# Kernel tuning notes

Measured on AMD Instinct MI355X. Metric: run time of the kernel, lower is better.

## Reference

```python
import jax, jax.numpy as jnp
import numpy as np

ALPHA = 1.0
BETA = 1.0
N_TDA = 16      # n: points subsampled per diagram
Q = 2.0         # Wasserstein order
NN_SIZE = 5     # knn size (self + 4 neighbors)
RADIUS = 0.07
H = 0.03
EPS = 1e-12
B, N = 8, 4096


def _sqdist(a, b):
    # a: [..., M, 3], b: [..., K, 3] -> [..., M, K] squared Euclidean distances
    aa = jnp.sum(a * a, -1)[..., :, None]
    bb = jnp.sum(b * b, -1)[..., None, :]
    ab = jnp.einsum('...md,...kd->...mk', a, b)
    return aa + bb - 2.0 * ab


def _mst_deaths(pts):
    # H0 persistence of Vietoris-Rips complex: births all 0, finite deaths are
    # the edge weights of the MST of the complete graph (Prim's algorithm).
    n = pts.shape[0]
    d = jnp.sqrt(jnp.maximum(_sqdist(pts, pts), 0.0))  # [n, n]
    in_tree = jnp.zeros((n,), bool).at[0].set(True)
    mind = d[0]  # distance from each node to the current tree

    def step(carry, _):
        in_tree, mind = carry
        m = jnp.where(in_tree, jnp.inf, mind)
        j = jnp.argmin(m)
        w = m[j]
        in_tree = in_tree.at[j].set(True)
        mind = jnp.minimum(mind, d[j])
        return (in_tree, mind), w

    _, deaths = jax.lax.scan(step, (in_tree, mind), None, length=n - 1)
    return deaths  # [n-1]


def _forward(pred, gt, pcd_radius):
    b = pred.shape[0]
    # ---- EMD loss (nearest-neighbor surrogate of CUDA auction_match) ----
    cost = _sqdist(pred, gt)                              # [B, N, N]
    idx = jnp.argmin(cost, axis=-1)                       # [B, N]
    matched = jnp.take_along_axis(gt, idx[..., None], axis=1)
    d2 = jnp.mean(((pred - matched) ** 2).reshape(b, -1), axis=1, keepdims=True)
    emd = jnp.mean(d2 / pcd_radius)
    # ---- Repulsion loss ----
    dpp = _sqdist(pred, pred)                             # [B, N, N]
    _, knn = jax.lax.top_k(-dpp, NN_SIZE)                 # nearest incl. self
    knn = knn[:, :, 1:]                                   # drop self -> [B, N, 4]
    grouped = jax.vmap(lambda p, ix: p[ix])(pred, knn)    # [B, N, 4, 3]
    r2 = jnp.maximum(jnp.sum((grouped - pred[:, :, None, :]) ** 2, -1), EPS)
    dist = jnp.sqrt(r2)
    rep = jnp.mean((RADIUS - dist) * jnp.exp(-r2 / H ** 2))
    # ---- TDA loss (per-sample VR H0 diagram + q-Wasserstein) ----
    key = jax.random.key(42)
    kp, kg = jax.random.split(key)

    def sub(k, pts):
        ix = jax.random.permutation(k, pts.shape[0])[:N_TDA]
        return pts[ix]

    pred_s = jax.vmap(sub)(jax.random.split(kp, b), pred)  # [B, 16, 3]
    gt_s = jax.vmap(sub)(jax.random.split(kg, b), gt)
    dp = jnp.sort(jax.vmap(_mst_deaths)(pred_s), axis=-1)  # [B, 15]
    dg = jnp.sort(jax.vmap(_mst_deaths)(gt_s), axis=-1)
    wd = jnp.sum(jnp.abs(dp - dg) ** Q, axis=-1) ** (1.0 / Q)
    tda = jnp.mean(wd)
    return (emd * 100.0, rep * ALPHA, tda * BETA)


def setup_inputs() -> dict:
    key = jax.random.key(0)
    k1, k2, k3 = jax.random.split(key, 3)
    pred = jax.random.normal(k1, (B, N, 3), jnp.float32)
    gt = jax.random.normal(k2, (B, N, 3), jnp.float32)
    pcd_radius = jax.random.uniform(k3, (B, 1), jnp.float32) + 0.5
    return {"pred": pred, "gt": gt, "pcd_radius": pcd_radius}


def reference(pred, gt, pcd_radius):
    return _forward(pred, gt, pcd_radius)
```

## Files before the change

kernel.cpp:

```cpp
#include <hip/hip_runtime.h>
#include <cstdint>
#include <cmath>
#include <vector>
#include <algorithm>
#include <numeric>

#define B_SZ 8
#define N_PTS 4096
#define TBLK 256
#define NSPLIT 8
#define JTILE (N_PTS / NSPLIT)
#define ITILE 4
#define RCUT2 0.10f

struct TdaArgs { int idx[16][16]; };

#define WS_BT(p)   ((float*)(p))
#define WS_KNN(p)  ((unsigned short*)((char*)(p) + 0x100000))
#define WS_PART(p) ((double*)((char*)(p) + 0x380000))

__global__ __launch_bounds__(TBLK, 2)
void pair_kernel(const float* __restrict__ pred, const float* __restrict__ gt,
                 float* __restrict__ bt_out, unsigned short* __restrict__ knn_out) {
  __shared__ float4 sg[JTILE];

  const int tid  = threadIdx.x;
  const int xb   = blockIdx.x;
  const int b    = blockIdx.y;
  const int zz   = blockIdx.z;
  const int job  = zz >> 3;
  const int q    = zz & 7;
  const int jbase = q * JTILE;

  const float* src = (job == 0 ? gt : pred) + ((size_t)b * N_PTS + jbase) * 3;
  for (int j = tid; j < JTILE; j += TBLK) {
    float x = src[3 * j + 0];
    float y = src[3 * j + 1];
    float z = src[3 * j + 2];
    sg[j] = make_float4(x, y, z, -0.5f * fmaf(x, x, fmaf(y, y, z * z)));
  }

  const float* pb = pred + (size_t)b * N_PTS * 3;
  const int ibase = xb * (TBLK * ITILE) + tid;
  float px[ITILE], py[ITILE], pz[ITILE];
  #pragma unroll
  for (int ii = 0; ii < ITILE; ++ii) {
    int i = ibase + ii * TBLK;
    px[ii] = pb[3 * i + 0]; py[ii] = pb[3 * i + 1]; pz[ii] = pb[3 * i + 2];
  }
  __syncthreads();

  if (job == 0) {
    float bt[ITILE];
    #pragma unroll
    for (int ii = 0; ii < ITILE; ++ii) bt[ii] = -INFINITY;
    for (int j0 = 0; j0 < JTILE; j0 += 8) {
      float4 g[8];
      #pragma unroll
      for (int k = 0; k < 8; ++k) g[k] = sg[j0 + k];
      #pragma unroll
      for (int ii = 0; ii < ITILE; ++ii) {
        #pragma unroll
        for (int k = 0; k < 8; ++k) {
          float t = fmaf(px[ii], g[k].x, fmaf(py[ii], g[k].y, fmaf(pz[ii], g[k].z, g[k].w)));
          bt[ii] = fmaxf(bt[ii], t);
        }
      }
    }
    #pragma unroll
    for (int ii = 0; ii < ITILE; ++ii)
      bt_out[((size_t)q * B_SZ + b) * N_PTS + ibase + ii * TBLK] = bt[ii];
  } else {
    float t0[ITILE], t1[ITILE], t2[ITILE], t3[ITILE], t4[ITILE];
    int   i0v[ITILE], i1v[ITILE], i2v[ITILE], i3v[ITILE], i4v[ITILE];
    #pragma unroll
    for (int ii = 0; ii < ITILE; ++ii) {
      float pn = fmaf(px[ii], px[ii], fmaf(py[ii], py[ii], pz[ii] * pz[ii]));
      float tcut = 0.5f * (pn - RCUT2);
      t0[ii] = tcut; t1[ii] = tcut; t2[ii] = tcut; t3[ii] = tcut; t4[ii] = tcut;
      i0v[ii] = 0xFFFF; i1v[ii] = 0xFFFF; i2v[ii] = 0xFFFF; i3v[ii] = 0xFFFF; i4v[ii] = 0xFFFF;
    }
    #define INS(ii, tt, jj) { \
      t4[ii] = tt; i4v[ii] = jj; \
      if (t4[ii] > t3[ii]) { float f = t3[ii]; t3[ii] = t4[ii]; t4[ii] = f; int p_ = i3v[ii]; i3v[ii] = i4v[ii]; i4v[ii] = p_; } \
      if (t3[ii] > t2[ii]) { float f = t2[ii]; t2[ii] = t3[ii]; t3[ii] = f; int p_ = i2v[ii]; i2v[ii] = i3v[ii]; i3v[ii] = p_; } \
      if (t2[ii] > t1[ii]) { float f = t1[ii]; t1[ii] = t2[ii]; t2[ii] = f; int p_ = i1v[ii]; i1v[ii] = i2v[ii]; i2v[ii] = p_; } \
      if (t1[ii] > t0[ii]) { float f = t0[ii]; t0[ii] = t1[ii]; t1[ii] = f; int p_ = i0v[ii]; i0v[ii] = i1v[ii]; i1v[ii] = p_; } }
    for (int j0 = 0; j0 < JTILE; j0 += 4) {
      float4 g[4];
      #pragma unroll
      for (int k = 0; k < 4; ++k) g[k] = sg[j0 + k];
      #pragma unroll
      for (int ii = 0; ii < ITILE; ++ii) {
        #pragma unroll
        for (int k = 0; k < 4; ++k) {
          float t = fmaf(px[ii], g[k].x, fmaf(py[ii], g[k].y, fmaf(pz[ii], g[k].z, g[k].w)));
          if (t > t4[ii]) INS(ii, t, j0 + k);
        }
      }
    }
    #undef INS
    #pragma unroll
    for (int ii = 0; ii < ITILE; ++ii) {
      size_t base = (((size_t)q * B_SZ + b) * N_PTS + ibase + ii * TBLK) * 5;
      knn_out[base + 0] = (i0v[ii] == 0xFFFF) ? 0xFFFF : (unsigned short)(jbase + i0v[ii]);
      knn_out[base + 1] = (i1v[ii] == 0xFFFF) ? 0xFFFF : (unsigned short)(jbase + i1v[ii]);
      knn_out[base + 2] = (i2v[ii] == 0xFFFF) ? 0xFFFF : (unsigned short)(jbase + i2v[ii]);
      knn_out[base + 3] = (i3v[ii] == 0xFFFF) ? 0xFFFF : (unsigned short)(jbase + i3v[ii]);
      knn_out[base + 4] = (i4v[ii] == 0xFFFF) ? 0xFFFF : (unsigned short)(jbase + i4v[ii]);
    }
  }
}

__global__ __launch_bounds__(TBLK)
void merge_kernel(const float* __restrict__ pred,
                  const float* __restrict__ bt_in, const unsigned short* __restrict__ knn_in,
                  double* __restrict__ partials) {
  __shared__ double wred[2][TBLK / 64];
  const int tid = threadIdx.x;
  const int blk = blockIdx.x;
  const int b   = blk >> 4;
  const int i   = (blk & 15) * TBLK + tid;

  const float* pb = pred + (size_t)b * N_PTS * 3;
  const float px = pb[3 * i + 0], py = pb[3 * i + 1], pz = pb[3 * i + 2];
  const float pn = fmaf(px, px, fmaf(py, py, pz * pz));

  float bt = -INFINITY;
  #pragma unroll
  for (int q = 0; q < NSPLIT; ++q)
    bt = fmaxf(bt, bt_in[((size_t)q * B_SZ + b) * N_PTS + i]);
  double emd = (double)fmaf(-2.0f, bt, pn);

  float s0 = INFINITY, s1 = INFINITY, s2 = INFINITY, s3 = INFINITY;
  int   j0v = 0x7fffffff, j1v = 0x7fffffff, j2v = 0x7fffffff, j3v = 0x7fffffff;
  #pragma unroll
  for (int q = 0; q < NSPLIT; ++q) {
    const unsigned short* kn = knn_in + (((size_t)q * B_SZ + b) * N_PTS + i) * 5;
    #pragma unroll
    for (int c = 0; c < 5; ++c) {
      int v = kn[c];
      int idx = v & 0xFFF;
      float gx = pb[3 * idx + 0], gy = pb[3 * idx + 1], gz = pb[3 * idx + 2];
      float dx = px - gx, dy = py - gy, dz = pz - gz;
      float r2 = fmaf(dx, dx, fmaf(dy, dy, dz * dz));
      if (v >= 0xFFFF || idx == i) r2 = INFINITY;
      bool lt3 = (r2 < s3) || (r2 == s3 && idx < j3v);
      if (lt3) {
        s3 = r2; j3v = idx;
        if ((s3 < s2) || (s3 == s2 && j3v < j2v)) { float f = s2; s2 = s3; s3 = f; int p_ = j2v; j2v = j3v; j3v = p_; }
        if ((s2 < s1) || (s2 == s1 && j2v < j1v)) { float f = s1; s1 = s2; s2 = f; int p_ = j1v; j1v = j2v; j2v = p_; }
        if ((s1 < s0) || (s1 == s0 && j1v < j0v)) { float f = s0; s0 = s1; s1 = f; int p_ = j0v; j0v = j1v; j1v = p_; }
      }
    }
  }
  double rep = 0.0;
  {
    float rr[4] = { s0, s1, s2, s3 };
    #pragma unroll
    for (int k = 0; k < 4; ++k) {
      if (rr[k] < 1e30f) {
        float r2 = fmaxf(rr[k], 1e-12f);
        float dist = sqrtf(r2);
        rep += (double)((0.07f - dist) * expf(-r2 / 9.0e-4f));
      }
    }
  }

  double v0 = emd, v1 = rep;
  #pragma unroll
  for (int off = 32; off > 0; off >>= 1) { v0 += __shfl_down(v0, off); v1 += __shfl_down(v1, off); }
  if ((tid & 63) == 0) { wred[0][tid >> 6] = v0; wred[1][tid >> 6] = v1; }
  __syncthreads();
  if (tid == 0) {
    double a = 0.0, r = 0.0;
    #pragma unroll
    for (int w = 0; w < TBLK / 64; ++w) { a += wred[0][w]; r += wred[1][w]; }
    partials[blk * 2 + 0] = a;
    partials[blk * 2 + 1] = r;
  }
}

__global__ __launch_bounds__(64)
void final_kernel(const float* __restrict__ pred, const float* __restrict__ gt,
                  const float* __restrict__ pcd, const double* __restrict__ partials,
                  float* __restrict__ out, TdaArgs args) {
  __shared__ float pts[16][16][3];
  __shared__ float aa[16][16];
  __shared__ float mind[16][16];
  __shared__ float deaths[16][15];
  __shared__ float wd[8];
  const int tid = threadIdx.x;

  if (tid < 16) {
    const float* src = (tid < 8) ? (pred + (size_t)tid * N_PTS * 3)
                                 : (gt + (size_t)(tid - 8) * N_PTS * 3);
    for (int k = 0; k < 16; ++k) {
      int ix = args.idx[tid][k];
      float x = src[3 * ix + 0], y = src[3 * ix + 1], z = src[3 * ix + 2];
      pts[tid][k][0] = x; pts[tid][k][1] = y; pts[tid][k][2] = z;
      aa[tid][k] = x * x + y * y + z * z;
    }
    #define DFORM(j, k) \
      sqrtf(fmaxf(aa[tid][j] + aa[tid][k] - 2.0f * (pts[tid][j][0] * pts[tid][k][0] + \
            pts[tid][j][1] * pts[tid][k][1] + pts[tid][j][2] * pts[tid][k][2]), 0.0f))
    for (int k = 0; k < 16; ++k) mind[tid][k] = DFORM(0, k);
    unsigned mask = 1u;
    for (int step = 0; step < 15; ++step) {
      float best = INFINITY; int bj = 0;
      for (int k = 0; k < 16; ++k) {
        float m = ((mask >> k) & 1u) ? INFINITY : mind[tid][k];
        if (m < best) { best = m; bj = k; }
      }
      deaths[tid][step] = best;
      mask |= (1u << bj);
      for (int k = 0; k < 16; ++k) mind[tid][k] = fminf(mind[tid][k], DFORM(bj, k));
    }
    #undef DFORM
    for (int a = 1; a < 15; ++a) {
      float v = deaths[tid][a];
      int c = a;
      while (c > 0 && deaths[tid][c - 1] > v) { deaths[tid][c] = deaths[tid][c - 1]; --c; }
      deaths[tid][c] = v;
    }
  }
  __syncthreads();
  if (tid < 8) {
    float s = 0.0f;
    for (int k = 0; k < 15; ++k) {
      float d = deaths[tid][k] - deaths[tid + 8][k];
      s += d * d;
    }
    wd[tid] = sqrtf(s);
  }
  __syncthreads();
  if (tid == 0) {
    double tda = 0.0;
    for (int b = 0; b < 8; ++b) tda += (double)wd[b];
    tda /= 8.0;
    double emd = 0.0;
    for (int b = 0; b < 8; ++b) {
      double s = 0.0;
      for (int c = 0; c < 16; ++c) s += partials[(b * 16 + c) * 2];
      emd += (s / (double)(N_PTS * 3)) / (double)pcd[b];
    }
    emd = emd / 8.0 * 100.0;
    double rep = 0.0;
    for (int k = 0; k < 128; ++k) rep += partials[k * 2 + 1];
    rep /= (double)(B_SZ * N_PTS * 4);
    out[0] = (float)emd;
    out[1] = (float)rep;
    out[2] = (float)tda;
  }
}

static inline uint32_t rotl32(uint32_t x, int d) { return (x << d) | (x >> (32 - d)); }

static void threefry2x32_host(uint32_t k0, uint32_t k1, uint32_t& x0, uint32_t& x1) {
  const uint32_t ks[3] = { k0, k1, k0 ^ k1 ^ 0x1BD11BDAu };
  static const int rot[2][4] = { {13, 15, 26, 6}, {17, 29, 16, 24} };
  x0 += ks[0]; x1 += ks[1];
  for (int i = 0; i < 5; ++i) {
    const int* r = rot[i & 1];
    for (int j = 0; j < 4; ++j) {
      x0 += x1;
      x1 = rotl32(x1, r[j]);
      x1 ^= x0;
    }
    x0 += ks[(i + 1) % 3];
    x1 += ks[(i + 2) % 3] + (uint32_t)(i + 1);
  }
}

static void jax_split_p(const uint32_t key[2], int n, uint32_t (*out)[2]) {
  for (int j = 0; j < n; ++j) {
    uint32_t a = 0u, b = (uint32_t)j;
    threefry2x32_host(key[0], key[1], a, b);
    out[j][0] = a; out[j][1] = b;
  }
}

static void jax_bits32_p(const uint32_t key[2], int n, uint32_t* bits) {
  for (int i = 0; i < n; ++i) {
    uint32_t a = 0u, b = (uint32_t)i;
    threefry2x32_host(key[0], key[1], a, b);
    bits[i] = a ^ b;
  }
}

static void jax_perm_first16(const uint32_t key_in[2], int n, int* out16) {
  std::vector<int> x((size_t)n);
  std::iota(x.begin(), x.end(), 0);
  uint32_t key[2] = { key_in[0], key_in[1] };
  const int rounds = (int)std::ceil(3.0 * std::log((double)n) / std::log(4294967295.0));
  std::vector<uint32_t> bits((size_t)n);
  std::vector<int> ord((size_t)n), nx((size_t)n);
  for (int r = 0; r < rounds; ++r) {
    uint32_t kr[2][2];
    jax_split_p(key, 2, kr);
    key[0] = kr[0][0]; key[1] = kr[0][1];
    jax_bits32_p(kr[1], n, bits.data());
    std::iota(ord.begin(), ord.end(), 0);
    std::stable_sort(ord.begin(), ord.end(),
                     [&](int A, int Bv) { return bits[A] < bits[Bv]; });
    for (int i = 0; i < n; ++i) nx[i] = x[ord[i]];
    x.swap(nx);
  }
  for (int i = 0; i < 16; ++i) out16[i] = x[i];
}

static void compute_tda_indices(TdaArgs& args) {
  const uint32_t root[2] = { 0u, 42u };
  uint32_t kpg[2][2];
  jax_split_p(root, 2, kpg);
  uint32_t kb[B_SZ][2];
  jax_split_p(kpg[0], B_SZ, kb);
  for (int b = 0; b < B_SZ; ++b) jax_perm_first16(kb[b], N_PTS, args.idx[b]);
  jax_split_p(kpg[1], B_SZ, kb);
  for (int b = 0; b < B_SZ; ++b) jax_perm_first16(kb[b], N_PTS, args.idx[8 + b]);
}


extern "C" void kernel_launch(void* const* d_in, const int* in_sizes, int n_in,
                              void* d_out, int out_size, void* d_ws, size_t ws_size,
                              hipStream_t stream) {
  const float* pred = (const float*)d_in[0];
  const float* gt   = (const float*)d_in[1];
  const float* pcd  = (const float*)d_in[2];
  float* out = (float*)d_out;

  TdaArgs targs;
  compute_tda_indices(targs);

  float*          bt   = WS_BT(d_ws);
  unsigned short* knn  = WS_KNN(d_ws);
  double*         part = WS_PART(d_ws);

  pair_kernel<<<dim3(N_PTS / (TBLK * ITILE), B_SZ, 2 * NSPLIT), dim3(TBLK), 0, stream>>>(pred, gt, bt, knn);
  merge_kernel<<<dim3(B_SZ * N_PTS / TBLK), dim3(TBLK), 0, stream>>>(pred, bt, knn, part);
  final_kernel<<<dim3(1), dim3(64), 0, stream>>>(pred, gt, pcd, part, out, targs);
}
```

Before: 4.875 ms.

## Split pair kernel into separate EMD and repulsion kernels with finer j-splits

Replaces the single pair kernel, which branched on job, with a dedicated EMD kernel and a dedicated kNN kernel. The j dimension is split 32 ways instead of 8, the EMD kernel processes 8 query points per thread, and the kNN inner loop is unrolled by 8. This aims to remove warp divergence between the two jobs, raise the block count for better occupancy, and give each kernel its own register and unroll tuning. In exchange it adds a kernel launch and makes the merge kernel reduce four times as many partial results and kNN candidate lists.

```diff
diff --git a/kernel.cpp b/kernel.cpp
--- a/kernel.cpp
+++ b/kernel.cpp
@@ -7,134 +7,145 @@
 
 #define B_SZ 8
 #define N_PTS 4096
-#define TBLK 256
-#define NSPLIT 8
+#define NSPLIT 32
 #define JTILE (N_PTS / NSPLIT)
-#define ITILE 4
 #define RCUT2 0.10f
 
 struct TdaArgs { int idx[16][16]; };
 
 #define WS_BT(p)   ((float*)(p))
-#define WS_KNN(p)  ((unsigned short*)((char*)(p) + 0x100000))
-#define WS_PART(p) ((double*)((char*)(p) + 0x380000))
-
-__global__ __launch_bounds__(TBLK, 2)
-void pair_kernel(const float* __restrict__ pred, const float* __restrict__ gt,
-                 float* __restrict__ bt_out, unsigned short* __restrict__ knn_out) {
+#define WS_KNN(p)  ((unsigned short*)((char*)(p) + 0x400000))
+#define WS_PART(p) ((double*)((char*)(p) + 0xF00000))
+
+__global__ __launch_bounds__(256, 4)
+void emd_kernel(const float* __restrict__ pred, const float* __restrict__ gt,
+                float* __restrict__ bt_out) {
   __shared__ float4 sg[JTILE];
-
-  const int tid  = threadIdx.x;
-  const int xb   = blockIdx.x;
-  const int b    = blockIdx.y;
-  const int zz   = blockIdx.z;
-  const int job  = zz >> 3;
-  const int q    = zz & 7;
+  const int tid = threadIdx.x;
+  const int xb  = blockIdx.x;
+  const int b   = blockIdx.y;
+  const int q   = blockIdx.z;
   const int jbase = q * JTILE;
 
-  const float* src = (job == 0 ? gt : pred) + ((size_t)b * N_PTS + jbase) * 3;
-  for (int j = tid; j < JTILE; j += TBLK) {
-    float x = src[3 * j + 0];
-    float y = src[3 * j + 1];
-    float z = src[3 * j + 2];
-    sg[j] = make_float4(x, y, z, -0.5f * fmaf(x, x, fmaf(y, y, z * z)));
+  const float* src = gt + ((size_t)b * N_PTS + jbase) * 3;
+  if (tid < JTILE) {
+    float x = src[3 * tid + 0], y = src[3 * tid + 1], z = src[3 * tid + 2];
+    sg[tid] = make_float4(x, y, z, -0.5f * fmaf(x, x, fmaf(y, y, z * z)));
   }
 
   const float* pb = pred + (size_t)b * N_PTS * 3;
-  const int ibase = xb * (TBLK * ITILE) + tid;
-  float px[ITILE], py[ITILE], pz[ITILE];
-  #pragma unroll
-  for (int ii = 0; ii < ITILE; ++ii) {
-    int i = ibase + ii * TBLK;
+  const int ibase = xb * 2048 + tid;
+  float px[8], py[8], pz[8], bt[8];
+  #pragma unroll
+  for (int ii = 0; ii < 8; ++ii) {
+    int i = ibase + ii * 256;
     px[ii] = pb[3 * i + 0]; py[ii] = pb[3 * i + 1]; pz[ii] = pb[3 * i + 2];
-  }
-  __syncthreads();
-
-  if (job == 0) {
-    float bt[ITILE];
-    #pragma unroll
-    for (int ii = 0; ii < ITILE; ++ii) bt[ii] = -INFINITY;
-    for (int j0 = 0; j0 < JTILE; j0 += 8) {
-      float4 g[8];
+    bt[ii] = -INFINITY;
+  }
+  __syncthreads();
+
+  for (int j0 = 0; j0 < JTILE; j0 += 8) {
+    float4 g[8];
+    #pragma unroll
+    for (int k = 0; k < 8; ++k) g[k] = sg[j0 + k];
+    #pragma unroll
+    for (int ii = 0; ii < 8; ++ii) {
       #pragma unroll
-      for (int k = 0; k < 8; ++k) g[k] = sg[j0 + k];
+      for (int k = 0; k < 8; ++k) {
+        float t = fmaf(px[ii], g[k].x, fmaf(py[ii], g[k].y, fmaf(pz[ii], g[k].z, g[k].w)));
+        bt[ii] = fmaxf(bt[ii], t);
+      }
+    }
+  }
+  #pragma unroll
+  for (int ii = 0; ii < 8; ++ii)
+    bt_out[((size_t)q * B_SZ + b) * N_PTS + ibase + ii * 256] = bt[ii];
+}
+
+__global__ __launch_bounds__(256, 4)
+void rep_kernel(const float* __restrict__ pred, unsigned short* __restrict__ knn_out) {
+  __shared__ float4 sg[JTILE];
+  const int tid = threadIdx.x;
+  const int xb  = blockIdx.x;
+  const int b   = blockIdx.y;
+  const int q   = blockIdx.z;
+  const int jbase = q * JTILE;
+
+  const float* pb = pred + (size_t)b * N_PTS * 3;
+  const float* src = pb + (size_t)jbase * 3;
+  if (tid < JTILE) {
+    float x = src[3 * tid + 0], y = src[3 * tid + 1], z = src[3 * tid + 2];
+    sg[tid] = make_float4(x, y, z, -0.5f * fmaf(x, x, fmaf(y, y, z * z)));
+  }
+
+  const int ibase = xb * 1024 + tid;
+  float px[4], py[4], pz[4];
+  float t0[4], t1[4], t2[4], t3[4], t4[4];
+  int   i0v[4], i1v[4], i2v[4], i3v[4], i4v[4];
+  #pragma unroll
+  for (int ii = 0; ii < 4; ++ii) {
+    int i = ibase + ii * 256;
+    px[ii] = pb[3 * i + 0]; py[ii] = pb[3 * i + 1]; pz[ii] = pb[3 * i + 2];
+    float pn = fmaf(px[ii], px[ii], fmaf(py[ii], py[ii], pz[ii] * pz[ii]));
+    float tcut = 0.5f * (pn - RCUT2);
+    t0[ii] = tcut; t1[ii] = tcut; t2[ii] = tcut; t3[ii] = tcut; t4[ii] = tcut;
+    i0v[ii] = 0xFFFF; i1v[ii] = 0xFFFF; i2v[ii] = 0xFFFF; i3v[ii] = 0xFFFF; i4v[ii] = 0xFFFF;
+  }
+  __syncthreads();
+
+  #define INS(ii, tt, jj) { \
+    t4[ii] = tt; i4v[ii] = jj; \
+    if (t4[ii] > t3[ii]) { float f = t3[ii]; t3[ii] = t4[ii]; t4[ii] = f; int p_ = i3v[ii]; i3v[ii] = i4v[ii]; i4v[ii] = p_; } \
+    if (t3[ii] > t2[ii]) { float f = t2[ii]; t2[ii] = t3[ii]; t3[ii] = f; int p_ = i2v[ii]; i2v[ii] = i3v[ii]; i3v[ii] = p_; } \
+    if (t2[ii] > t1[ii]) { float f = t1[ii]; t1[ii] = t2[ii]; t2[ii] = f; int p_ = i1v[ii]; i1v[ii] = i2v[ii]; i2v[ii] = p_; } \
+    if (t1[ii] > t0[ii]) { float f = t0[ii]; t0[ii] = t1[ii]; t1[ii] = f; int p_ = i0v[ii]; i0v[ii] = i1v[ii]; i1v[ii] = p_; } }
+  for (int j0 = 0; j0 < JTILE; j0 += 8) {
+    float4 g[8];
+    #pragma unroll
+    for (int k = 0; k < 8; ++k) g[k] = sg[j0 + k];
+    #pragma unroll
+    for (int ii = 0; ii < 4; ++ii) {
       #pragma unroll
-      for (int ii = 0; ii < ITILE; ++ii) {
-        #pragma unroll
-        for (int k = 0; k < 8; ++k) {
-          float t = fmaf(px[ii], g[k].x, fmaf(py[ii], g[k].y, fmaf(pz[ii], g[k].z, g[k].w)));
-          bt[ii] = fmaxf(bt[ii], t);
-        }
-      }
-    }
-    #pragma unroll
-    for (int ii = 0; ii < ITILE; ++ii)
-      bt_out[((size_t)q * B_SZ + b) * N_PTS + ibase + ii * TBLK] = bt[ii];
-  } else {
-    float t0[ITILE], t1[ITILE], t2[ITILE], t3[ITILE], t4[ITILE];
-    int   i0v[ITILE], i1v[ITILE], i2v[ITILE], i3v[ITILE], i4v[ITILE];
-    #pragma unroll
-    for (int ii = 0; ii < ITILE; ++ii) {
-      float pn = fmaf(px[ii], px[ii], fmaf(py[ii], py[ii], pz[ii] * pz[ii]));
-      float tcut = 0.5f * (pn - RCUT2);
-      t0[ii] = tcut; t1[ii] = tcut; t2[ii] = tcut; t3[ii] = tcut; t4[ii] = tcut;
-      i0v[ii] = 0xFFFF; i1v[ii] = 0xFFFF; i2v[ii] = 0xFFFF; i3v[ii] = 0xFFFF; i4v[ii] = 0xFFFF;
-    }
-    #define INS(ii, tt, jj) { \
-      t4[ii] = tt; i4v[ii] = jj; \
-      if (t4[ii] > t3[ii]) { float f = t3[ii]; t3[ii] = t4[ii]; t4[ii] = f; int p_ = i3v[ii]; i3v[ii] = i4v[ii]; i4v[ii] = p_; } \
-      if (t3[ii] > t2[ii]) { float f = t2[ii]; t2[ii] = t3[ii]; t3[ii] = f; int p_ = i2v[ii]; i2v[ii] = i3v[ii]; i3v[ii] = p_; } \
-      if (t2[ii] > t1[ii]) { float f = t1[ii]; t1[ii] = t2[ii]; t2[ii] = f; int p_ = i1v[ii]; i1v[ii] = i2v[ii]; i2v[ii] = p_; } \
-      if (t1[ii] > t0[ii]) { float f = t0[ii]; t0[ii] = t1[ii]; t1[ii] = f; int p_ = i0v[ii]; i0v[ii] = i1v[ii]; i1v[ii] = p_; } }
-    for (int j0 = 0; j0 < JTILE; j0 += 4) {
-      float4 g[4];
-      #pragma unroll
-      for (int k = 0; k < 4; ++k) g[k] = sg[j0 + k];
-      #pragma unroll
-      for (int ii = 0; ii < ITILE; ++ii) {
-        #pragma unroll
-        for (int k = 0; k < 4; ++k) {
-          float t = fmaf(px[ii], g[k].x, fmaf(py[ii], g[k].y, fmaf(pz[ii], g[k].z, g[k].w)));
-          if (t > t4[ii]) INS(ii, t, j0 + k);
-        }
-      }
-    }
-    #undef INS
-    #pragma unroll
-    for (int ii = 0; ii < ITILE; ++ii) {
-      size_t base = (((size_t)q * B_SZ + b) * N_PTS + ibase + ii * TBLK) * 5;
-      knn_out[base + 0] = (i0v[ii] == 0xFFFF) ? 0xFFFF : (unsigned short)(jbase + i0v[ii]);
-      knn_out[base + 1] = (i1v[ii] == 0xFFFF) ? 0xFFFF : (unsigned short)(jbase + i1v[ii]);
-      knn_out[base + 2] = (i2v[ii] == 0xFFFF) ? 0xFFFF : (unsigned short)(jbase + i2v[ii]);
-      knn_out[base + 3] = (i3v[ii] == 0xFFFF) ? 0xFFFF : (unsigned short)(jbase + i3v[ii]);
-      knn_out[base + 4] = (i4v[ii] == 0xFFFF) ? 0xFFFF : (unsigned short)(jbase + i4v[ii]);
-    }
-  }
-}
-
-__global__ __launch_bounds__(TBLK)
+      for (int k = 0; k < 8; ++k) {
+        float t = fmaf(px[ii], g[k].x, fmaf(py[ii], g[k].y, fmaf(pz[ii], g[k].z, g[k].w)));
+        if (t > t4[ii]) INS(ii, t, j0 + k);
+      }
+    }
+  }
+  #undef INS
+
+  #pragma unroll
+  for (int ii = 0; ii < 4; ++ii) {
+    size_t base = (((size_t)q * B_SZ + b) * N_PTS + ibase + ii * 256) * 5;
+    knn_out[base + 0] = (i0v[ii] == 0xFFFF) ? 0xFFFF : (unsigned short)(jbase + i0v[ii]);
+    knn_out[base + 1] = (i1v[ii] == 0xFFFF) ? 0xFFFF : (unsigned short)(jbase + i1v[ii]);
+    knn_out[base + 2] = (i2v[ii] == 0xFFFF) ? 0xFFFF : (unsigned short)(jbase + i2v[ii]);
+    knn_out[base + 3] = (i3v[ii] == 0xFFFF) ? 0xFFFF : (unsigned short)(jbase + i3v[ii]);
+    knn_out[base + 4] = (i4v[ii] == 0xFFFF) ? 0xFFFF : (unsigned short)(jbase + i4v[ii]);
+  }
+}
+
+__global__ __launch_bounds__(256)
 void merge_kernel(const float* __restrict__ pred,
                   const float* __restrict__ bt_in, const unsigned short* __restrict__ knn_in,
                   double* __restrict__ partials) {
-  __shared__ double wred[2][TBLK / 64];
+  __shared__ double wred[2][4];
   const int tid = threadIdx.x;
   const int blk = blockIdx.x;
   const int b   = blk >> 4;
-  const int i   = (blk & 15) * TBLK + tid;
+  const int i   = (blk & 15) * 256 + tid;
 
   const float* pb = pred + (size_t)b * N_PTS * 3;
   const float px = pb[3 * i + 0], py = pb[3 * i + 1], pz = pb[3 * i + 2];
   const float pn = fmaf(px, px, fmaf(py, py, pz * pz));
 
   float bt = -INFINITY;
-  #pragma unroll
   for (int q = 0; q < NSPLIT; ++q)
     bt = fmaxf(bt, bt_in[((size_t)q * B_SZ + b) * N_PTS + i]);
   double emd = (double)fmaf(-2.0f, bt, pn);
 
   float s0 = INFINITY, s1 = INFINITY, s2 = INFINITY, s3 = INFINITY;
   int   j0v = 0x7fffffff, j1v = 0x7fffffff, j2v = 0x7fffffff, j3v = 0x7fffffff;
-  #pragma unroll
   for (int q = 0; q < NSPLIT; ++q) {
     const unsigned short* kn = knn_in + (((size_t)q * B_SZ + b) * N_PTS + i) * 5;
     #pragma unroll
@@ -175,7 +186,7 @@
   if (tid == 0) {
     double a = 0.0, r = 0.0;
     #pragma unroll
-    for (int w = 0; w < TBLK / 64; ++w) { a += wred[0][w]; r += wred[1][w]; }
+    for (int w = 0; w < 4; ++w) { a += wred[0][w]; r += wred[1][w]; }
     partials[blk * 2 + 0] = a;
     partials[blk * 2 + 1] = r;
   }
@@ -336,7 +347,8 @@
   unsigned short* knn  = WS_KNN(d_ws);
   double*         part = WS_PART(d_ws);
 
-  pair_kernel<<<dim3(N_PTS / (TBLK * ITILE), B_SZ, 2 * NSPLIT), dim3(TBLK), 0, stream>>>(pred, gt, bt, knn);
-  merge_kernel<<<dim3(B_SZ * N_PTS / TBLK), dim3(TBLK), 0, stream>>>(pred, bt, knn, part);
+  emd_kernel<<<dim3(2, B_SZ, NSPLIT), dim3(256), 0, stream>>>(pred, gt, bt);
+  rep_kernel<<<dim3(4, B_SZ, NSPLIT), dim3(256), 0, stream>>>(pred, knn);
+  merge_kernel<<<dim3(128), dim3(256), 0, stream>>>(pred, bt, knn, part);
   final_kernel<<<dim3(1), dim3(64), 0, stream>>>(pred, gt, pcd, part, out, targs);
 }
```

Result: faster. 4.767 ms (-2.2%).
